# Performance work log

Measured on AMD Instinct MI355X. Metric: run time of the kernel, lower is better.

Reference implementation:

```python
import jax, jax.numpy as jnp
import numpy as np

L, B, S, H, O, IN = 8, 512, 128, 1024, 1024, 1024


def setup_inputs() -> dict:
    key = jax.random.key(0)
    ks = jax.random.split(key, 16)
    x = jax.random.normal(ks[0], (B, S, IN), dtype=jnp.float32)
    h_prev = jnp.zeros((L, B, H), dtype=jnp.float32)
    def w(k, shape):
        return jax.random.normal(k, shape, dtype=jnp.float32) * 0.01
    # input_size == hidden_size, so all layers stack into [L, ., .]
    W_xz = w(ks[1], (L, H, H)); W_hz = w(ks[2], (L, H, H)); b_z = jnp.zeros((L, H), jnp.float32)
    W_xr = w(ks[3], (L, H, H)); W_hr = w(ks[4], (L, H, H)); b_r = jnp.zeros((L, H), jnp.float32)
    W_xh = w(ks[5], (L, H, H)); W_hh = w(ks[6], (L, H, H)); b_h = jnp.zeros((L, H), jnp.float32)
    W_hy = w(ks[7], (H, O)); b_y = jnp.zeros((O,), jnp.float32)
    return {"x": x, "h_prev": h_prev, "W_xz": W_xz, "W_hz": W_hz, "b_z": b_z,
            "W_xr": W_xr, "W_hr": W_hr, "b_r": b_r, "W_xh": W_xh, "W_hh": W_hh,
            "b_h": b_h, "W_hy": W_hy, "b_y": b_y}


def reference(x, h_prev, W_xz, W_hz, b_z, W_xr, W_hr, b_r, W_xh, W_hh, b_h, W_hy, b_y):
    # Faithful to source: timestep loop runs over num_layers (= L) steps (source bug kept).
    nlayers = W_xz.shape[0]
    h = [h_prev[l] for l in range(nlayers)]  # per-layer hidden state [B, H]
    outputs, h_seq = [], []
    for t in range(nlayers):
        inp = x[:, t, :]
        for l in range(nlayers):
            hp = h[l]
            z = jax.nn.sigmoid(inp @ W_xz[l] + hp @ W_hz[l] + b_z[l])
            r = jax.nn.sigmoid(inp @ W_xr[l] + hp @ W_hr[l] + b_r[l])
            # note: (r * hp) @ W_hh matches python operator precedence in source
            h_tilde = jnp.tanh(inp @ W_xh[l] + (r * hp) @ W_hh[l] + b_h[l])
            h[l] = (1.0 - z) * hp + z * h_tilde
            inp = h[l]  # next layer sees this timestep's updated state
        outputs.append(h[-1] @ W_hy + b_y)
        h_seq.append(jnp.stack(h, axis=0))
    outputs = jnp.stack(outputs, axis=1)          # [B, T, O]
    h_seq_stacked = jnp.stack(h_seq, axis=1)      # [L, T, B, H]
    h_current = jnp.stack(h, axis=0)              # [L, B, H]
    return outputs, h_seq_stacked, h_current
```

## Files before the change

### kernel.cpp

```cpp
#include <hip/hip_runtime.h>
#include <hip/hip_bf16.h>

typedef __bf16 bf16;
typedef __attribute__((ext_vector_type(8))) __bf16 bf16x8;
typedef __attribute__((ext_vector_type(4))) float f32x4;

constexpr int kH = 1024;
constexpr int kB = 512;
constexpr int kT = 8;
constexpr int kL = 8;
constexpr int kS = 128;

constexpr int BM = 64, BN = 128, BK = 32;
constexpr int LDA = BK + 8;
constexpr int LDB = BK + 8;

__device__ __forceinline__ float sigmoidf_(float v) { return 1.0f / (1.0f + __expf(-v)); }

__device__ __forceinline__ int xcd_swizzle(int g, int nwg) {
  int q = nwg >> 3, r = nwg & 7;
  int xcd = g & 7, idx = g >> 3;
  return (xcd < r ? xcd * (q + 1) : r * (q + 1) + (xcd - r) * q) + idx;
}

__device__ __forceinline__ bf16x8 cvt8(float4 a, float4 b) {
  bf16x8 o;
  o[0] = (bf16)a.x; o[1] = (bf16)a.y; o[2] = (bf16)a.z; o[3] = (bf16)a.w;
  o[4] = (bf16)b.x; o[5] = (bf16)b.y; o[6] = (bf16)b.z; o[7] = (bf16)b.w;
  return o;
}

__global__ __launch_bounds__(256) void wconv_kernel(
    const float* __restrict__ Wxz, const float* __restrict__ Whz,
    const float* __restrict__ Wxr, const float* __restrict__ Whr,
    const float* __restrict__ Wxh, const float* __restrict__ Whh,
    const float* __restrict__ Why, bf16* __restrict__ wt) {
  __shared__ float tile[64][65];
  int mat = blockIdx.z;
  const float* src;
  if (mat < 48) {
    int g = mat >> 3;
    const float* bases[6] = {Wxz, Whz, Wxr, Whr, Wxh, Whh};
    src = bases[g] + (size_t)(mat & 7) * kH * kH;
  } else {
    src = Why;
  }
  bf16* dst = wt + (size_t)mat * kH * kH;
  int k0 = blockIdx.x * 64;
  int n0 = blockIdx.y * 64;
  int tid = threadIdx.x;
  int cl = (tid & 15) * 4;
  int rw = tid >> 4;
#pragma unroll
  for (int i = 0; i < 4; ++i) {
    int r = rw + i * 16;
    float4 v = *(const float4*)(src + (size_t)(k0 + r) * kH + n0 + cl);
    tile[r][cl] = v.x; tile[r][cl + 1] = v.y; tile[r][cl + 2] = v.z; tile[r][cl + 3] = v.w;
  }
  __syncthreads();
#pragma unroll
  for (int p = 0; p < 2; ++p) {
    int idx = p * 256 + tid;
    int n = idx >> 3;
    int koff = (idx & 7) * 8;
    bf16x8 o;
#pragma unroll
    for (int i = 0; i < 8; ++i) o[i] = (bf16)tile[koff + i][n];
    *(bf16x8*)(dst + (size_t)(n0 + n) * kH + k0 + koff) = o;
  }
}

__global__ __launch_bounds__(256, 2) void gru_phase1(
    const float* __restrict__ x, const float* __restrict__ hprev,
    const float* __restrict__ hseq, const bf16* __restrict__ wt,
    const float* __restrict__ b_z, const float* __restrict__ b_r,
    float* __restrict__ Zs, float* __restrict__ C1s, bf16* __restrict__ RHs,
    int diag, int t_lo) {
  int w = xcd_swizzle(blockIdx.x, gridDim.x);
  int bm0 = (w & 7) * BM;
  int bn0 = ((w >> 3) & 7) * BN;
  int cell = w >> 6;
  int t = t_lo + cell;
  int l = diag - t;
  const float* inp; int inp_stride;
  if (l == 0) { inp = x + (size_t)t * kH; inp_stride = kS * kH; }
  else        { inp = hseq + ((size_t)((l - 1) * kT + t)) * kB * kH; inp_stride = kH; }
  const float* hp = (t == 0) ? hprev + (size_t)l * kB * kH
                             : hseq + ((size_t)(l * kT + (t - 1))) * kB * kH;
  const bf16* Wp[5];
#pragma unroll
  for (int g = 0; g < 5; ++g) Wp[g] = wt + ((size_t)g * 8 + l) * kH * kH;
  float* Zc  = Zs  + (size_t)cell * kB * kH;
  float* C1c = C1s + (size_t)cell * kB * kH;
  bf16*  RHc = RHs + (size_t)cell * kB * kH;

  __shared__ bf16 sInp[BM * LDA];
  __shared__ bf16 sHp[BM * LDA];
  __shared__ bf16 sB[5][BN * LDB];

  int tid = threadIdx.x;
  int lane = tid & 63;
  int wv = tid >> 6;

  f32x4 zacc[4][2] = {};
  f32x4 racc[4][2] = {};
  f32x4 cacc[4][2] = {};

  int sr = tid >> 2;
  int sc = (tid & 3) * 8;

  for (int k0 = 0; k0 < kH; k0 += BK) {
    {
      const float* pi = inp + (size_t)(bm0 + sr) * inp_stride + k0 + sc;
      float4 a0 = *(const float4*)pi;
      float4 a1 = *(const float4*)(pi + 4);
      *(bf16x8*)&sInp[sr * LDA + sc] = cvt8(a0, a1);
      const float* ph = hp + (size_t)(bm0 + sr) * kH + k0 + sc;
      float4 h0 = *(const float4*)ph;
      float4 h1 = *(const float4*)(ph + 4);
      *(bf16x8*)&sHp[sr * LDA + sc] = cvt8(h0, h1);
    }
#pragma unroll
    for (int g = 0; g < 5; ++g) {
#pragma unroll
      for (int p = 0; p < 2; ++p) {
        int idx = p * 256 + tid;
        int r = idx >> 2;
        int c = (idx & 3) * 8;
        *(bf16x8*)&sB[g][r * LDB + c] =
            *(const bf16x8*)(Wp[g] + (size_t)(bn0 + r) * kH + k0 + c);
      }
    }
    __syncthreads();
    int frow = lane & 15;
    int fk = (lane >> 4) * 8;
    bf16x8 ai[4], ah[4];
#pragma unroll
    for (int m = 0; m < 4; ++m) {
      ai[m] = *(const bf16x8*)&sInp[(m * 16 + frow) * LDA + fk];
      ah[m] = *(const bf16x8*)&sHp[(m * 16 + frow) * LDA + fk];
    }
#pragma unroll
    for (int nf = 0; nf < 2; ++nf) {
      int nr = wv * 32 + nf * 16 + frow;
      bf16x8 bxz = *(const bf16x8*)&sB[0][nr * LDB + fk];
      bf16x8 bhz = *(const bf16x8*)&sB[1][nr * LDB + fk];
      bf16x8 bxr = *(const bf16x8*)&sB[2][nr * LDB + fk];
      bf16x8 bhr = *(const bf16x8*)&sB[3][nr * LDB + fk];
      bf16x8 bxh = *(const bf16x8*)&sB[4][nr * LDB + fk];
#pragma unroll
      for (int m = 0; m < 4; ++m) {
        zacc[m][nf] = __builtin_amdgcn_mfma_f32_16x16x32_bf16(ai[m], bxz, zacc[m][nf], 0, 0, 0);
        zacc[m][nf] = __builtin_amdgcn_mfma_f32_16x16x32_bf16(ah[m], bhz, zacc[m][nf], 0, 0, 0);
        racc[m][nf] = __builtin_amdgcn_mfma_f32_16x16x32_bf16(ai[m], bxr, racc[m][nf], 0, 0, 0);
        racc[m][nf] = __builtin_amdgcn_mfma_f32_16x16x32_bf16(ah[m], bhr, racc[m][nf], 0, 0, 0);
        cacc[m][nf] = __builtin_amdgcn_mfma_f32_16x16x32_bf16(ai[m], bxh, cacc[m][nf], 0, 0, 0);
      }
    }
    __syncthreads();
  }
  int frow = lane & 15;
  int rbase = (lane >> 4) * 4;
#pragma unroll
  for (int m = 0; m < 4; ++m) {
#pragma unroll
    for (int nf = 0; nf < 2; ++nf) {
      int gcol = bn0 + wv * 32 + nf * 16 + frow;
      float bz = b_z[l * kH + gcol];
      float br = b_r[l * kH + gcol];
#pragma unroll
      for (int q = 0; q < 4; ++q) {
        int grow = bm0 + m * 16 + rbase + q;
        size_t off = (size_t)grow * kH + gcol;
        float z = sigmoidf_(zacc[m][nf][q] + bz);
        float r = sigmoidf_(racc[m][nf][q] + br);
        float hpv = hp[off];
        Zc[off] = z;
        C1c[off] = cacc[m][nf][q];
        RHc[off] = (bf16)(r * hpv);
      }
    }
  }
}

__global__ __launch_bounds__(256, 2) void gru_phase2(
    const float* __restrict__ hprev, float* __restrict__ hseq,
    float* __restrict__ hcur, const bf16* __restrict__ wt,
    const float* __restrict__ b_h, const float* __restrict__ Zs,
    const float* __restrict__ C1s, const bf16* __restrict__ RHs,
    int diag, int t_lo) {
  int w = xcd_swizzle(blockIdx.x, gridDim.x);
  int bm0 = (w & 7) * BM;
  int bn0 = ((w >> 3) & 7) * BN;
  int cell = w >> 6;
  int t = t_lo + cell;
  int l = diag - t;
  const bf16* Whh = wt + ((size_t)5 * 8 + l) * kH * kH;
  const float* hp = (t == 0) ? hprev + (size_t)l * kB * kH
                             : hseq + ((size_t)(l * kT + (t - 1))) * kB * kH;
  float* hout = hseq + ((size_t)(l * kT + t)) * kB * kH;
  const float* Zc  = Zs  + (size_t)cell * kB * kH;
  const float* C1c = C1s + (size_t)cell * kB * kH;
  const bf16*  RHc = RHs + (size_t)cell * kB * kH;

  __shared__ bf16 sA[BM * LDA];
  __shared__ bf16 sB[BN * LDB];

  int tid = threadIdx.x;
  int lane = tid & 63;
  int wv = tid >> 6;

  f32x4 acc[4][2] = {};
  int sr = tid >> 2;
  int sc = (tid & 3) * 8;

  for (int k0 = 0; k0 < kH; k0 += BK) {
    *(bf16x8*)&sA[sr * LDA + sc] = *(const bf16x8*)(RHc + (size_t)(bm0 + sr) * kH + k0 + sc);
#pragma unroll
    for (int p = 0; p < 2; ++p) {
      int idx = p * 256 + tid;
      int r = idx >> 2;
      int c = (idx & 3) * 8;
      *(bf16x8*)&sB[r * LDB + c] = *(const bf16x8*)(Whh + (size_t)(bn0 + r) * kH + k0 + c);
    }
    __syncthreads();
    int frow = lane & 15;
    int fk = (lane >> 4) * 8;
    bf16x8 a[4];
#pragma unroll
    for (int m = 0; m < 4; ++m) a[m] = *(const bf16x8*)&sA[(m * 16 + frow) * LDA + fk];
#pragma unroll
    for (int nf = 0; nf < 2; ++nf) {
      int nr = wv * 32 + nf * 16 + frow;
      bf16x8 b = *(const bf16x8*)&sB[nr * LDB + fk];
#pragma unroll
      for (int m = 0; m < 4; ++m)
        acc[m][nf] = __builtin_amdgcn_mfma_f32_16x16x32_bf16(a[m], b, acc[m][nf], 0, 0, 0);
    }
    __syncthreads();
  }
  int frow = lane & 15;
  int rbase = (lane >> 4) * 4;
  bool last = (t == kT - 1);
#pragma unroll
  for (int m = 0; m < 4; ++m) {
#pragma unroll
    for (int nf = 0; nf < 2; ++nf) {
      int gcol = bn0 + wv * 32 + nf * 16 + frow;
      float bh = b_h[l * kH + gcol];
#pragma unroll
      for (int q = 0; q < 4; ++q) {
        int grow = bm0 + m * 16 + rbase + q;
        size_t off = (size_t)grow * kH + gcol;
        float ht = tanhf(acc[m][nf][q] + C1c[off] + bh);
        float z = Zc[off];
        float hn = (1.0f - z) * hp[off] + z * ht;
        hout[off] = hn;
        if (last) hcur[(size_t)l * kB * kH + off] = hn;
      }
    }
  }
}

__global__ __launch_bounds__(256, 2) void out_gemm(
    const float* __restrict__ h7, const bf16* __restrict__ WhyT,
    const float* __restrict__ b_y, float* __restrict__ out) {
  __shared__ bf16 sA[BM * LDA];
  __shared__ bf16 sB[BN * LDB];
  int w = xcd_swizzle(blockIdx.x, gridDim.x);
  int bm0 = (w & 63) * BM;
  int bn0 = (w >> 6) * BN;
  int tid = threadIdx.x;
  int lane = tid & 63;
  int wv = tid >> 6;
  f32x4 acc[4][2] = {};
  int sr = tid >> 2;
  int sc = (tid & 3) * 8;
  for (int k0 = 0; k0 < kH; k0 += BK) {
    const float* pa = h7 + (size_t)(bm0 + sr) * kH + k0 + sc;
    float4 a0 = *(const float4*)pa;
    float4 a1 = *(const float4*)(pa + 4);
    *(bf16x8*)&sA[sr * LDA + sc] = cvt8(a0, a1);
#pragma unroll
    for (int p = 0; p < 2; ++p) {
      int idx = p * 256 + tid;
      int r = idx >> 2;
      int c = (idx & 3) * 8;
      *(bf16x8*)&sB[r * LDB + c] = *(const bf16x8*)(WhyT + (size_t)(bn0 + r) * kH + k0 + c);
    }
    __syncthreads();
    int frow = lane & 15;
    int fk = (lane >> 4) * 8;
    bf16x8 a[4];
#pragma unroll
    for (int m = 0; m < 4; ++m) a[m] = *(const bf16x8*)&sA[(m * 16 + frow) * LDA + fk];
#pragma unroll
    for (int nf = 0; nf < 2; ++nf) {
      int nr = wv * 32 + nf * 16 + frow;
      bf16x8 b = *(const bf16x8*)&sB[nr * LDB + fk];
#pragma unroll
      for (int m = 0; m < 4; ++m)
        acc[m][nf] = __builtin_amdgcn_mfma_f32_16x16x32_bf16(a[m], b, acc[m][nf], 0, 0, 0);
    }
    __syncthreads();
  }
  int frow = lane & 15;
  int rbase = (lane >> 4) * 4;
#pragma unroll
  for (int m = 0; m < 4; ++m) {
#pragma unroll
    for (int nf = 0; nf < 2; ++nf) {
      int gcol = bn0 + wv * 32 + nf * 16 + frow;
      float by = b_y[gcol];
#pragma unroll
      for (int q = 0; q < 4; ++q) {
        int grow = bm0 + m * 16 + rbase + q;
        int tt = grow >> 9;
        int bb = grow & 511;
        out[((size_t)bb * kT + tt) * kH + gcol] = acc[m][nf][q] + by;
      }
    }
  }
}

extern "C" void kernel_launch(void* const* d_in, const int* in_sizes, int n_in,
                              void* d_out, int out_size, void* d_ws, size_t ws_size,
                              hipStream_t stream) {
  const float* x     = (const float*)d_in[0];
  const float* hprev = (const float*)d_in[1];
  const float* Wxz   = (const float*)d_in[2];
  const float* Whz   = (const float*)d_in[3];
  const float* bz    = (const float*)d_in[4];
  const float* Wxr   = (const float*)d_in[5];
  const float* Whr   = (const float*)d_in[6];
  const float* br    = (const float*)d_in[7];
  const float* Wxh   = (const float*)d_in[8];
  const float* Whh   = (const float*)d_in[9];
  const float* bh    = (const float*)d_in[10];
  const float* Why   = (const float*)d_in[11];
  const float* by    = (const float*)d_in[12];

  float* out  = (float*)d_out;
  float* hseq = out + (size_t)kB * kT * kH;
  float* hcur = hseq + (size_t)kL * kT * kB * kH;

  bf16* wt = (bf16*)d_ws;
  char* p = (char*)d_ws + (size_t)49 * kH * kH * 2;
  float* Zs  = (float*)p; p += (size_t)8 * kB * kH * 4;
  float* C1s = (float*)p; p += (size_t)8 * kB * kH * 4;
  bf16*  RHs = (bf16*)p;

  wconv_kernel<<<dim3(16, 16, 49), 256, 0, stream>>>(Wxz, Whz, Wxr, Whr, Wxh, Whh, Why, wt);

  for (int dg = 0; dg <= 14; ++dg) {
    int t_lo = dg > 7 ? dg - 7 : 0;
    int t_hi = dg < 7 ? dg : 7;
    int nc = t_hi - t_lo + 1;
    gru_phase1<<<dim3(64 * nc), 256, 0, stream>>>(x, hprev, hseq, wt, bz, br, Zs, C1s, RHs, dg, t_lo);
    gru_phase2<<<dim3(64 * nc), 256, 0, stream>>>(hprev, hseq, hcur, wt, bh, Zs, C1s, RHs, dg, t_lo);
  }

  out_gemm<<<dim3(512), 256, 0, stream>>>(hseq + (size_t)7 * kT * kB * kH,
                                          wt + (size_t)48 * kH * kH, by, out);
}
```

Measured before the change: 1.649 ms.

## Restructure GRU kernels with concatenated-K bf16 GEMMs and async LDS staging

Replaces the two-phase GRU kernels with a z/r kernel and a candidate kernel. Each treats [inp|h] against a concatenated 2048-K weight, with the z and r gates split across blocks. Inputs and hidden states are pre-converted to bf16 buffers, tiles grow to 128x128x64, staging uses global_load_lds, intermediates are stored in bf16, and the C1 buffer is dropped by moving the Wxh product into the second kernel. The aim is to cut fp32 load and convert traffic and increase MFMA reuse per tile. The cost is fewer blocks per diagonal (lower occupancy on small diagonals), LDS bank conflicts from the unpadded layout, and more bf16 rounding.

```diff
diff --git a/kernel.cpp b/kernel.cpp
--- a/kernel.cpp
+++ b/kernel.cpp
@@ -3,6 +3,7 @@
 
 typedef __bf16 bf16;
 typedef __attribute__((ext_vector_type(8))) __bf16 bf16x8;
+typedef __attribute__((ext_vector_type(4))) __bf16 bf16x4;
 typedef __attribute__((ext_vector_type(4))) float f32x4;
 
 constexpr int kH = 1024;
@@ -10,10 +11,9 @@
 constexpr int kT = 8;
 constexpr int kL = 8;
 constexpr int kS = 128;
-
-constexpr int BM = 64, BN = 128, BK = 32;
-constexpr int LDA = BK + 8;
-constexpr int LDB = BK + 8;
+constexpr size_t SL = (size_t)kB * kH;
+
+constexpr int BM = 128, BN = 128, BK = 64;
 
 __device__ __forceinline__ float sigmoidf_(float v) { return 1.0f / (1.0f + __expf(-v)); }
 
@@ -23,29 +23,79 @@
   return (xcd < r ? xcd * (q + 1) : r * (q + 1) + (xcd - r) * q) + idx;
 }
 
-__device__ __forceinline__ bf16x8 cvt8(float4 a, float4 b) {
-  bf16x8 o;
-  o[0] = (bf16)a.x; o[1] = (bf16)a.y; o[2] = (bf16)a.z; o[3] = (bf16)a.w;
-  o[4] = (bf16)b.x; o[5] = (bf16)b.y; o[6] = (bf16)b.z; o[7] = (bf16)b.w;
-  return o;
-}
-
-__global__ __launch_bounds__(256) void wconv_kernel(
+__device__ __forceinline__ void stage_tile(const bf16* __restrict__ src, int stride,
+                                           bf16* lds, int tid) {
+#pragma unroll
+  for (int i = 0; i < 4; ++i) {
+    int seg = i * 256 + tid;
+    int row = seg >> 3;
+    int c8 = (seg & 7) * 8;
+    __builtin_amdgcn_global_load_lds(
+        (const __attribute__((address_space(1))) void*)(src + (size_t)row * stride + c8),
+        (__attribute__((address_space(3))) void*)(lds + seg * 8),
+        16, 0, 0);
+  }
+}
+
+__device__ __forceinline__ void mma_step(const bf16* sA, const bf16* sB,
+                                         f32x4 acc[4][4], int lane, int wr, int wc) {
+  int frow = lane & 15, fko = (lane >> 4) * 8;
+#pragma unroll
+  for (int kk = 0; kk < 2; ++kk) {
+    bf16x8 a[4], b[4];
+#pragma unroll
+    for (int m = 0; m < 4; ++m)
+      a[m] = *(const bf16x8*)&sA[(wr * 64 + m * 16 + frow) * BK + kk * 32 + fko];
+#pragma unroll
+    for (int n = 0; n < 4; ++n)
+      b[n] = *(const bf16x8*)&sB[(wc * 64 + n * 16 + frow) * BK + kk * 32 + fko];
+#pragma unroll
+    for (int m = 0; m < 4; ++m)
+#pragma unroll
+      for (int n = 0; n < 4; ++n)
+        acc[m][n] = __builtin_amdgcn_mfma_f32_16x16x32_bf16(a[m], b[n], acc[m][n], 0, 0, 0);
+  }
+}
+
+__global__ __launch_bounds__(256) void cvt_inputs(
+    const float* __restrict__ x, const float* __restrict__ hprev,
+    bf16* __restrict__ xb, bf16* __restrict__ hpb) {
+  size_t i = ((size_t)blockIdx.x * 256 + threadIdx.x) * 4;
+  if (blockIdx.y == 0) {
+    size_t t = i >> 19, r = i & (SL - 1), b = r >> 10, h = r & 1023;
+    float4 v = *(const float4*)(x + ((b * kS + t) << 10) + h);
+    bf16x4 o = {(bf16)v.x, (bf16)v.y, (bf16)v.z, (bf16)v.w};
+    *(bf16x4*)(xb + i) = o;
+  } else {
+    float4 v = *(const float4*)(hprev + i);
+    bf16x4 o = {(bf16)v.x, (bf16)v.y, (bf16)v.z, (bf16)v.w};
+    *(bf16x4*)(hpb + i) = o;
+  }
+}
+
+__global__ __launch_bounds__(256) void wconv(
     const float* __restrict__ Wxz, const float* __restrict__ Whz,
     const float* __restrict__ Wxr, const float* __restrict__ Whr,
     const float* __restrict__ Wxh, const float* __restrict__ Whh,
-    const float* __restrict__ Why, bf16* __restrict__ wt) {
+    const float* __restrict__ Why, bf16* __restrict__ wzr,
+    bf16* __restrict__ wch, bf16* __restrict__ wy) {
   __shared__ float tile[64][65];
   int mat = blockIdx.z;
   const float* src;
+  bf16* dst;
+  size_t dstride;
   if (mat < 48) {
-    int g = mat >> 3;
+    int g = mat >> 3, l = mat & 7;
     const float* bases[6] = {Wxz, Whz, Wxr, Whr, Wxh, Whh};
-    src = bases[g] + (size_t)(mat & 7) * kH * kH;
+    src = bases[g] + (size_t)l * kH * kH;
+    int pair = g >> 1;
+    int koff = (g & 1) * 1024;
+    if (pair < 2) dst = wzr + ((size_t)(pair * 8 + l)) * kH * 2048 + koff;
+    else          dst = wch + (size_t)l * kH * 2048 + koff;
+    dstride = 2048;
   } else {
-    src = Why;
-  }
-  bf16* dst = wt + (size_t)mat * kH * kH;
+    src = Why; dst = wy; dstride = 1024;
+  }
   int k0 = blockIdx.x * 64;
   int n0 = blockIdx.y * 64;
   int tid = threadIdx.x;
@@ -62,262 +112,168 @@
   for (int p = 0; p < 2; ++p) {
     int idx = p * 256 + tid;
     int n = idx >> 3;
-    int koff = (idx & 7) * 8;
+    int ko = (idx & 7) * 8;
     bf16x8 o;
 #pragma unroll
-    for (int i = 0; i < 8; ++i) o[i] = (bf16)tile[koff + i][n];
-    *(bf16x8*)(dst + (size_t)(n0 + n) * kH + k0 + koff) = o;
-  }
-}
-
-__global__ __launch_bounds__(256, 2) void gru_phase1(
-    const float* __restrict__ x, const float* __restrict__ hprev,
-    const float* __restrict__ hseq, const bf16* __restrict__ wt,
+    for (int i = 0; i < 8; ++i) o[i] = (bf16)tile[ko + i][n];
+    *(bf16x8*)(dst + (size_t)(n0 + n) * dstride + k0 + ko) = o;
+  }
+}
+
+__global__ __launch_bounds__(256, 2) void gru_zr(
+    const bf16* __restrict__ xb, const bf16* __restrict__ hpb,
+    const bf16* __restrict__ hb, const float* __restrict__ hseq,
+    const float* __restrict__ hprevf, const bf16* __restrict__ wzr,
     const float* __restrict__ b_z, const float* __restrict__ b_r,
-    float* __restrict__ Zs, float* __restrict__ C1s, bf16* __restrict__ RHs,
-    int diag, int t_lo) {
+    bf16* __restrict__ Zs, bf16* __restrict__ RHs, int diag, int t_lo) {
+  __shared__ bf16 sA[BM * BK];
+  __shared__ bf16 sB[BN * BK];
   int w = xcd_swizzle(blockIdx.x, gridDim.x);
-  int bm0 = (w & 7) * BM;
-  int bn0 = ((w >> 3) & 7) * BN;
+  int bm0 = (w & 3) * BM;
+  int bn0 = ((w >> 2) & 7) * BN;
+  int gate = (w >> 5) & 1;
   int cell = w >> 6;
-  int t = t_lo + cell;
-  int l = diag - t;
-  const float* inp; int inp_stride;
-  if (l == 0) { inp = x + (size_t)t * kH; inp_stride = kS * kH; }
-  else        { inp = hseq + ((size_t)((l - 1) * kT + t)) * kB * kH; inp_stride = kH; }
-  const float* hp = (t == 0) ? hprev + (size_t)l * kB * kH
-                             : hseq + ((size_t)(l * kT + (t - 1))) * kB * kH;
-  const bf16* Wp[5];
-#pragma unroll
-  for (int g = 0; g < 5; ++g) Wp[g] = wt + ((size_t)g * 8 + l) * kH * kH;
-  float* Zc  = Zs  + (size_t)cell * kB * kH;
-  float* C1c = C1s + (size_t)cell * kB * kH;
-  bf16*  RHc = RHs + (size_t)cell * kB * kH;
-
-  __shared__ bf16 sInp[BM * LDA];
-  __shared__ bf16 sHp[BM * LDA];
-  __shared__ bf16 sB[5][BN * LDB];
-
-  int tid = threadIdx.x;
-  int lane = tid & 63;
-  int wv = tid >> 6;
-
-  f32x4 zacc[4][2] = {};
-  f32x4 racc[4][2] = {};
-  f32x4 cacc[4][2] = {};
-
-  int sr = tid >> 2;
-  int sc = (tid & 3) * 8;
-
-  for (int k0 = 0; k0 < kH; k0 += BK) {
-    {
-      const float* pi = inp + (size_t)(bm0 + sr) * inp_stride + k0 + sc;
-      float4 a0 = *(const float4*)pi;
-      float4 a1 = *(const float4*)(pi + 4);
-      *(bf16x8*)&sInp[sr * LDA + sc] = cvt8(a0, a1);
-      const float* ph = hp + (size_t)(bm0 + sr) * kH + k0 + sc;
-      float4 h0 = *(const float4*)ph;
-      float4 h1 = *(const float4*)(ph + 4);
-      *(bf16x8*)&sHp[sr * LDA + sc] = cvt8(h0, h1);
-    }
-#pragma unroll
-    for (int g = 0; g < 5; ++g) {
-#pragma unroll
-      for (int p = 0; p < 2; ++p) {
-        int idx = p * 256 + tid;
-        int r = idx >> 2;
-        int c = (idx & 3) * 8;
-        *(bf16x8*)&sB[g][r * LDB + c] =
-            *(const bf16x8*)(Wp[g] + (size_t)(bn0 + r) * kH + k0 + c);
+  int t = t_lo + cell, l = diag - t;
+  int pprev = (diag - 1) & 1;
+  const bf16* inpb = (l == 0) ? xb + (size_t)t * SL
+                              : hb + (size_t)(pprev * 8 + (l - 1)) * SL;
+  const bf16* hpbp = (t == 0) ? hpb + (size_t)l * SL
+                              : hb + (size_t)(pprev * 8 + l) * SL;
+  const float* hpf = (t == 0) ? hprevf + (size_t)l * SL
+                              : hseq + (size_t)(l * kT + t - 1) * SL;
+  const bf16* wB = wzr + (size_t)(gate * 8 + l) * kH * 2048;
+
+  int tid = threadIdx.x, lane = tid & 63, wv = tid >> 6;
+  int wr = wv >> 1, wc = wv & 1;
+  f32x4 acc[4][4] = {};
+
+  for (int k0 = 0; k0 < 2048; k0 += BK) {
+    const bf16* As = (k0 < 1024) ? inpb + (size_t)bm0 * kH + k0
+                                 : hpbp + (size_t)bm0 * kH + (k0 - 1024);
+    stage_tile(As, kH, sA, tid);
+    stage_tile(wB + (size_t)bn0 * 2048 + k0, 2048, sB, tid);
+    __syncthreads();
+    mma_step(sA, sB, acc, lane, wr, wc);
+    __syncthreads();
+  }
+
+  const float* bias = gate ? b_r : b_z;
+  int frow = lane & 15, rb = (lane >> 4) * 4;
+  bf16* Zc = Zs + (size_t)cell * SL;
+  bf16* RHc = RHs + (size_t)cell * SL;
+#pragma unroll
+  for (int n = 0; n < 4; ++n) {
+    int gcol = bn0 + wc * 64 + n * 16 + frow;
+    float bv = bias[l * kH + gcol];
+#pragma unroll
+    for (int m = 0; m < 4; ++m) {
+#pragma unroll
+      for (int q = 0; q < 4; ++q) {
+        int grow = bm0 + wr * 64 + m * 16 + rb + q;
+        size_t off = (size_t)grow * kH + gcol;
+        float v = sigmoidf_(acc[m][n][q] + bv);
+        if (gate == 0) Zc[off] = (bf16)v;
+        else           RHc[off] = (bf16)(v * hpf[off]);
       }
     }
-    __syncthreads();
-    int frow = lane & 15;
-    int fk = (lane >> 4) * 8;
-    bf16x8 ai[4], ah[4];
+  }
+}
+
+__global__ __launch_bounds__(256, 2) void gru_ch(
+    const bf16* __restrict__ xb, bf16* __restrict__ hb,
+    const float* __restrict__ hprevf, float* __restrict__ hseq,
+    float* __restrict__ hcur, bf16* __restrict__ hb7,
+    const bf16* __restrict__ wch, const float* __restrict__ b_h,
+    const bf16* __restrict__ Zs, const bf16* __restrict__ RHs,
+    int diag, int t_lo) {
+  __shared__ bf16 sA[BM * BK];
+  __shared__ bf16 sB[BN * BK];
+  int w = xcd_swizzle(blockIdx.x, gridDim.x);
+  int bm0 = (w & 3) * BM;
+  int bn0 = ((w >> 2) & 7) * BN;
+  int cell = w >> 5;
+  int t = t_lo + cell, l = diag - t;
+  int pprev = (diag - 1) & 1, pcur = diag & 1;
+  const bf16* inpb = (l == 0) ? xb + (size_t)t * SL
+                              : hb + (size_t)(pprev * 8 + (l - 1)) * SL;
+  const bf16* RHc = RHs + (size_t)cell * SL;
+  const bf16* Zc = Zs + (size_t)cell * SL;
+  const float* hpf = (t == 0) ? hprevf + (size_t)l * SL
+                              : hseq + (size_t)(l * kT + t - 1) * SL;
+  float* hout = hseq + (size_t)(l * kT + t) * SL;
+  bf16* hbout = hb + (size_t)(pcur * 8 + l) * SL;
+  const bf16* wB = wch + (size_t)l * kH * 2048;
+
+  int tid = threadIdx.x, lane = tid & 63, wv = tid >> 6;
+  int wr = wv >> 1, wc = wv & 1;
+  f32x4 acc[4][4] = {};
+
+  for (int k0 = 0; k0 < 2048; k0 += BK) {
+    const bf16* As = (k0 < 1024) ? inpb + (size_t)bm0 * kH + k0
+                                 : RHc + (size_t)bm0 * kH + (k0 - 1024);
+    stage_tile(As, kH, sA, tid);
+    stage_tile(wB + (size_t)bn0 * 2048 + k0, 2048, sB, tid);
+    __syncthreads();
+    mma_step(sA, sB, acc, lane, wr, wc);
+    __syncthreads();
+  }
+
+  int frow = lane & 15, rb = (lane >> 4) * 4;
+  bool lastT = (t == kT - 1);
+  bool lastL = (l == kL - 1);
+#pragma unroll
+  for (int n = 0; n < 4; ++n) {
+    int gcol = bn0 + wc * 64 + n * 16 + frow;
+    float bh = b_h[l * kH + gcol];
 #pragma unroll
     for (int m = 0; m < 4; ++m) {
-      ai[m] = *(const bf16x8*)&sInp[(m * 16 + frow) * LDA + fk];
-      ah[m] = *(const bf16x8*)&sHp[(m * 16 + frow) * LDA + fk];
-    }
-#pragma unroll
-    for (int nf = 0; nf < 2; ++nf) {
-      int nr = wv * 32 + nf * 16 + frow;
-      bf16x8 bxz = *(const bf16x8*)&sB[0][nr * LDB + fk];
-      bf16x8 bhz = *(const bf16x8*)&sB[1][nr * LDB + fk];
-      bf16x8 bxr = *(const bf16x8*)&sB[2][nr * LDB + fk];
-      bf16x8 bhr = *(const bf16x8*)&sB[3][nr * LDB + fk];
-      bf16x8 bxh = *(const bf16x8*)&sB[4][nr * LDB + fk];
-#pragma unroll
-      for (int m = 0; m < 4; ++m) {
-        zacc[m][nf] = __builtin_amdgcn_mfma_f32_16x16x32_bf16(ai[m], bxz, zacc[m][nf], 0, 0, 0);
-        zacc[m][nf] = __builtin_amdgcn_mfma_f32_16x16x32_bf16(ah[m], bhz, zacc[m][nf], 0, 0, 0);
-        racc[m][nf] = __builtin_amdgcn_mfma_f32_16x16x32_bf16(ai[m], bxr, racc[m][nf], 0, 0, 0);
-        racc[m][nf] = __builtin_amdgcn_mfma_f32_16x16x32_bf16(ah[m], bhr, racc[m][nf], 0, 0, 0);
-        cacc[m][nf] = __builtin_amdgcn_mfma_f32_16x16x32_bf16(ai[m], bxh, cacc[m][nf], 0, 0, 0);
+#pragma unroll
+      for (int q = 0; q < 4; ++q) {
+        int grow = bm0 + wr * 64 + m * 16 + rb + q;
+        size_t off = (size_t)grow * kH + gcol;
+        float ht = tanhf(acc[m][n][q] + bh);
+        float z = (float)Zc[off];
+        float hpv = hpf[off];
+        float hn = (1.0f - z) * hpv + z * ht;
+        hout[off] = hn;
+        hbout[off] = (bf16)hn;
+        if (lastL) hb7[(size_t)t * SL + off] = (bf16)hn;
+        if (lastT) hcur[(size_t)l * SL + off] = hn;
       }
     }
-    __syncthreads();
-  }
-  int frow = lane & 15;
-  int rbase = (lane >> 4) * 4;
-#pragma unroll
-  for (int m = 0; m < 4; ++m) {
-#pragma unroll
-    for (int nf = 0; nf < 2; ++nf) {
-      int gcol = bn0 + wv * 32 + nf * 16 + frow;
-      float bz = b_z[l * kH + gcol];
-      float br = b_r[l * kH + gcol];
+  }
+}
+
+__global__ __launch_bounds__(256, 2) void out_gemm(
+    const bf16* __restrict__ hb7, const bf16* __restrict__ wy,
+    const float* __restrict__ b_y, float* __restrict__ out) {
+  __shared__ bf16 sA[BM * BK];
+  __shared__ bf16 sB[BN * BK];
+  int w = xcd_swizzle(blockIdx.x, gridDim.x);
+  int bm0 = (w & 31) * BM;
+  int bn0 = (w >> 5) * BN;
+  int tid = threadIdx.x, lane = tid & 63, wv = tid >> 6;
+  int wr = wv >> 1, wc = wv & 1;
+  f32x4 acc[4][4] = {};
+  for (int k0 = 0; k0 < kH; k0 += BK) {
+    stage_tile(hb7 + (size_t)bm0 * kH + k0, kH, sA, tid);
+    stage_tile(wy + (size_t)bn0 * kH + k0, kH, sB, tid);
+    __syncthreads();
+    mma_step(sA, sB, acc, lane, wr, wc);
+    __syncthreads();
+  }
+  int frow = lane & 15, rb = (lane >> 4) * 4;
+#pragma unroll
+  for (int n = 0; n < 4; ++n) {
+    int gcol = bn0 + wc * 64 + n * 16 + frow;
+    float by = b_y[gcol];
+#pragma unroll
+    for (int m = 0; m < 4; ++m) {
 #pragma unroll
       for (int q = 0; q < 4; ++q) {
-        int grow = bm0 + m * 16 + rbase + q;
-        size_t off = (size_t)grow * kH + gcol;
-        float z = sigmoidf_(zacc[m][nf][q] + bz);
-        float r = sigmoidf_(racc[m][nf][q] + br);
-        float hpv = hp[off];
-        Zc[off] = z;
-        C1c[off] = cacc[m][nf][q];
-        RHc[off] = (bf16)(r * hpv);
-      }
-    }
-  }
-}
-
-__global__ __launch_bounds__(256, 2) void gru_phase2(
-    const float* __restrict__ hprev, float* __restrict__ hseq,
-    float* __restrict__ hcur, const bf16* __restrict__ wt,
-    const float* __restrict__ b_h, const float* __restrict__ Zs,
-    const float* __restrict__ C1s, const bf16* __restrict__ RHs,
-    int diag, int t_lo) {
-  int w = xcd_swizzle(blockIdx.x, gridDim.x);
-  int bm0 = (w & 7) * BM;
-  int bn0 = ((w >> 3) & 7) * BN;
-  int cell = w >> 6;
-  int t = t_lo + cell;
-  int l = diag - t;
-  const bf16* Whh = wt + ((size_t)5 * 8 + l) * kH * kH;
-  const float* hp = (t == 0) ? hprev + (size_t)l * kB * kH
-                             : hseq + ((size_t)(l * kT + (t - 1))) * kB * kH;
-  float* hout = hseq + ((size_t)(l * kT + t)) * kB * kH;
-  const float* Zc  = Zs  + (size_t)cell * kB * kH;
-  const float* C1c = C1s + (size_t)cell * kB * kH;
-  const bf16*  RHc = RHs + (size_t)cell * kB * kH;
-
-  __shared__ bf16 sA[BM * LDA];
-  __shared__ bf16 sB[BN * LDB];
-
-  int tid = threadIdx.x;
-  int lane = tid & 63;
-  int wv = tid >> 6;
-
-  f32x4 acc[4][2] = {};
-  int sr = tid >> 2;
-  int sc = (tid & 3) * 8;
-
-  for (int k0 = 0; k0 < kH; k0 += BK) {
-    *(bf16x8*)&sA[sr * LDA + sc] = *(const bf16x8*)(RHc + (size_t)(bm0 + sr) * kH + k0 + sc);
-#pragma unroll
-    for (int p = 0; p < 2; ++p) {
-      int idx = p * 256 + tid;
-      int r = idx >> 2;
-      int c = (idx & 3) * 8;
-      *(bf16x8*)&sB[r * LDB + c] = *(const bf16x8*)(Whh + (size_t)(bn0 + r) * kH + k0 + c);
-    }
-    __syncthreads();
-    int frow = lane & 15;
-    int fk = (lane >> 4) * 8;
-    bf16x8 a[4];
-#pragma unroll
-    for (int m = 0; m < 4; ++m) a[m] = *(const bf16x8*)&sA[(m * 16 + frow) * LDA + fk];
-#pragma unroll
-    for (int nf = 0; nf < 2; ++nf) {
-      int nr = wv * 32 + nf * 16 + frow;
-      bf16x8 b = *(const bf16x8*)&sB[nr * LDB + fk];
-#pragma unroll
-      for (int m = 0; m < 4; ++m)
-        acc[m][nf] = __builtin_amdgcn_mfma_f32_16x16x32_bf16(a[m], b, acc[m][nf], 0, 0, 0);
-    }
-    __syncthreads();
-  }
-  int frow = lane & 15;
-  int rbase = (lane >> 4) * 4;
-  bool last = (t == kT - 1);
-#pragma unroll
-  for (int m = 0; m < 4; ++m) {
-#pragma unroll
-    for (int nf = 0; nf < 2; ++nf) {
-      int gcol = bn0 + wv * 32 + nf * 16 + frow;
-      float bh = b_h[l * kH + gcol];
-#pragma unroll
-      for (int q = 0; q < 4; ++q) {
-        int grow = bm0 + m * 16 + rbase + q;
-        size_t off = (size_t)grow * kH + gcol;
-        float ht = tanhf(acc[m][nf][q] + C1c[off] + bh);
-        float z = Zc[off];
-        float hn = (1.0f - z) * hp[off] + z * ht;
-        hout[off] = hn;
-        if (last) hcur[(size_t)l * kB * kH + off] = hn;
-      }
-    }
-  }
-}
-
-__global__ __launch_bounds__(256, 2) void out_gemm(
-    const float* __restrict__ h7, const bf16* __restrict__ WhyT,
-    const float* __restrict__ b_y, float* __restrict__ out) {
-  __shared__ bf16 sA[BM * LDA];
-  __shared__ bf16 sB[BN * LDB];
-  int w = xcd_swizzle(blockIdx.x, gridDim.x);
-  int bm0 = (w & 63) * BM;
-  int bn0 = (w >> 6) * BN;
-  int tid = threadIdx.x;
-  int lane = tid & 63;
-  int wv = tid >> 6;
-  f32x4 acc[4][2] = {};
-  int sr = tid >> 2;
-  int sc = (tid & 3) * 8;
-  for (int k0 = 0; k0 < kH; k0 += BK) {
-    const float* pa = h7 + (size_t)(bm0 + sr) * kH + k0 + sc;
-    float4 a0 = *(const float4*)pa;
-    float4 a1 = *(const float4*)(pa + 4);
-    *(bf16x8*)&sA[sr * LDA + sc] = cvt8(a0, a1);
-#pragma unroll
-    for (int p = 0; p < 2; ++p) {
-      int idx = p * 256 + tid;
-      int r = idx >> 2;
-      int c = (idx & 3) * 8;
-      *(bf16x8*)&sB[r * LDB + c] = *(const bf16x8*)(WhyT + (size_t)(bn0 + r) * kH + k0 + c);
-    }
-    __syncthreads();
-    int frow = lane & 15;
-    int fk = (lane >> 4) * 8;
-    bf16x8 a[4];
-#pragma unroll
-    for (int m = 0; m < 4; ++m) a[m] = *(const bf16x8*)&sA[(m * 16 + frow) * LDA + fk];
-#pragma unroll
-    for (int nf = 0; nf < 2; ++nf) {
-      int nr = wv * 32 + nf * 16 + frow;
-      bf16x8 b = *(const bf16x8*)&sB[nr * LDB + fk];
-#pragma unroll
-      for (int m = 0; m < 4; ++m)
-        acc[m][nf] = __builtin_amdgcn_mfma_f32_16x16x32_bf16(a[m], b, acc[m][nf], 0, 0, 0);
-    }
-    __syncthreads();
-  }
-  int frow = lane & 15;
-  int rbase = (lane >> 4) * 4;
-#pragma unroll
-  for (int m = 0; m < 4; ++m) {
-#pragma unroll
-    for (int nf = 0; nf < 2; ++nf) {
-      int gcol = bn0 + wv * 32 + nf * 16 + frow;
-      float by = b_y[gcol];
-#pragma unroll
-      for (int q = 0; q < 4; ++q) {
-        int grow = bm0 + m * 16 + rbase + q;
-        int tt = grow >> 9;
-        int bb = grow & 511;
-        out[((size_t)bb * kT + tt) * kH + gcol] = acc[m][nf][q] + by;
+        int grow = bm0 + wr * 64 + m * 16 + rb + q;
+        int tt = grow >> 9, bb = grow & 511;
+        out[((size_t)bb * kT + tt) * kH + gcol] = acc[m][n][q] + by;
       }
     }
   }
@@ -344,22 +300,30 @@
   float* hseq = out + (size_t)kB * kT * kH;
   float* hcur = hseq + (size_t)kL * kT * kB * kH;
 
-  bf16* wt = (bf16*)d_ws;
-  char* p = (char*)d_ws + (size_t)49 * kH * kH * 2;
-  float* Zs  = (float*)p; p += (size_t)8 * kB * kH * 4;
-  float* C1s = (float*)p; p += (size_t)8 * kB * kH * 4;
-  bf16*  RHs = (bf16*)p;
-
-  wconv_kernel<<<dim3(16, 16, 49), 256, 0, stream>>>(Wxz, Whz, Wxr, Whr, Wxh, Whh, Why, wt);
+  char* p = (char*)d_ws;
+  bf16* wzr = (bf16*)p;            p += (size_t)2 * 8 * kH * 2048 * 2;
+  bf16* wch = (bf16*)p;            p += (size_t)8 * kH * 2048 * 2;
+  bf16* wy  = (bf16*)p;            p += (size_t)kH * kH * 2;
+  bf16* xb  = (bf16*)p;            p += (size_t)8 * SL * 2;
+  bf16* hpb = (bf16*)p;            p += (size_t)8 * SL * 2;
+  bf16* hb  = (bf16*)p;            p += (size_t)16 * SL * 2;
+  bf16* hb7 = (bf16*)p;            p += (size_t)8 * SL * 2;
+  bf16* Zs  = (bf16*)p;            p += (size_t)8 * SL * 2;
+  bf16* RHs = (bf16*)p;
+
+  cvt_inputs<<<dim3(4096, 2), 256, 0, stream>>>(x, hprev, xb, hpb);
+  wconv<<<dim3(16, 16, 49), 256, 0, stream>>>(Wxz, Whz, Wxr, Whr, Wxh, Whh, Why,
+                                              wzr, wch, wy);
 
   for (int dg = 0; dg <= 14; ++dg) {
     int t_lo = dg > 7 ? dg - 7 : 0;
     int t_hi = dg < 7 ? dg : 7;
     int nc = t_hi - t_lo + 1;
-    gru_phase1<<<dim3(64 * nc), 256, 0, stream>>>(x, hprev, hseq, wt, bz, br, Zs, C1s, RHs, dg, t_lo);
-    gru_phase2<<<dim3(64 * nc), 256, 0, stream>>>(hprev, hseq, hcur, wt, bh, Zs, C1s, RHs, dg, t_lo);
-  }
-
-  out_gemm<<<dim3(512), 256, 0, stream>>>(hseq + (size_t)7 * kT * kB * kH,
-                                          wt + (size_t)48 * kH * kH, by, out);
-}
+    gru_zr<<<dim3(nc * 64), 256, 0, stream>>>(xb, hpb, hb, hseq, hprev, wzr, bz, br,
+                                              Zs, RHs, dg, t_lo);
+    gru_ch<<<dim3(nc * 32), 256, 0, stream>>>(xb, hb, hprev, hseq, hcur, hb7,
+                                              wch, bh, Zs, RHs, dg, t_lo);
+  }
+
+  out_gemm<<<dim3(256), 256, 0, stream>>>(hb7, wy, by, out);
+}
```

After: 2.057 ms. +24.7%, slower.
